# Optimization experiments

Measured on AMD Instinct MI355X. Metric: run time of the kernel, lower is better.

Reference implementation:

```python
import jax, jax.numpy as jnp
import numpy as np

EPS = 1e-12  # F.normalize default eps

def _l2norm(x, axis):
    n = jnp.maximum(jnp.linalg.norm(x, axis=axis, keepdims=True), EPS)
    return x / n

def setup_inputs() -> dict:
    key = jax.random.key(0)
    k1, k2 = jax.random.split(key)
    B, G, D, K = 256, 100, 768, 128
    h = jax.random.normal(k1, (B, G, D), dtype=jnp.float32)
    duplicate_pooling = jax.random.normal(k2, (G, D, K), dtype=jnp.float32)
    out_extrap = jnp.zeros((B, G, K), dtype=jnp.float32)
    return {"h": h, "duplicate_pooling": duplicate_pooling, "out_extrap": out_extrap}

def reference(h, duplicate_pooling, out_extrap):
    # normalize=True: L2-normalize each h[:, i, :] over feature dim (dim=1 of the
    # flattened [B, D] view == last axis), and each w_i = W[i] over dim=0 (the D axis).
    hn = _l2norm(h, axis=-1)                       # [B, G, D]
    wn = _l2norm(duplicate_pooling, axis=1)        # [G, D, K]
    # Fused grouped batched GEMM over all G groups at once.
    out = jnp.einsum('bgd,gdk->bgk', hn, wn)       # [B, G, K]
    return out
```

## Files before the change

### kernel.cpp

```cpp
#include <hip/hip_runtime.h>

#define Gn   100
#define Bn   256
#define Dn   768
#define Kn   128
#define LDP  40

typedef __attribute__((ext_vector_type(8))) short short8;
typedef __attribute__((ext_vector_type(4))) float f32x4;

__device__ inline unsigned short f2b(float f) {
  union { float f; unsigned u; } v; v.f = f;
  unsigned r = v.u + 0x7FFFu + ((v.u >> 16) & 1u);
  return (unsigned short)(r >> 16);
}

__global__ __launch_bounds__(256) void groupfc_kernel(
    const float* __restrict__ h, const float* __restrict__ W,
    float* __restrict__ out) {
  const int g    = blockIdx.z;
  const int mt   = blockIdx.x;
  const int nt   = blockIdx.y;
  const int t    = threadIdx.x;
  const int lane = t & 63;
  const int wave = t >> 6;
  const int wm   = wave >> 1, wn = wave & 1;

  __shared__ short Alds[2][64 * LDP];
  __shared__ short Blds[2][64 * LDP];
  __shared__ float AssqL[64];
  __shared__ float BssqL[4][64];

  f32x4 acc00 = {0.f,0.f,0.f,0.f};
  f32x4 acc01 = acc00, acc10 = acc00, acc11 = acc00;

  const int ar = t >> 2;
  const int ac = (t & 3) * 8;
  const float* aptr = h + ((size_t)(mt * 64 + ar) * Gn + g) * Dn + ac;
  const int bk = t & 63;
  const int bd = (t >> 6) * 8;
  const float* bptr = W + (size_t)g * (Dn * Kn) + (size_t)bd * Kn + nt * 64 + bk;

  const int quad = lane >> 4;
  const int koff = quad * 8;
  const int l15  = lane & 15;
  const int m0   = wm * 32 + l15;
  const int n0   = wn * 32 + l15;

  float assq = 0.f, bssq = 0.f;

  float4 a0 = *(const float4*)(aptr);
  float4 a1 = *(const float4*)(aptr + 4);
  float bv[8];
#pragma unroll
  for (int i = 0; i < 8; ++i) bv[i] = bptr[(size_t)i * Kn];

  for (int kc = 0; kc < 24; ++kc) {
    float4 na0, na1;
    float nbv[8];
    if (kc < 23) {
      const int d0 = (kc + 1) * 32;
      na0 = *(const float4*)(aptr + d0);
      na1 = *(const float4*)(aptr + d0 + 4);
#pragma unroll
      for (int i = 0; i < 8; ++i) nbv[i] = bptr[(size_t)(d0 + i) * Kn];
    }

    assq += a0.x*a0.x + a0.y*a0.y + a0.z*a0.z + a0.w*a0.w
          + a1.x*a1.x + a1.y*a1.y + a1.z*a1.z + a1.w*a1.w;
    union { unsigned short us[8]; short8 v; } pa;
    pa.us[0]=f2b(a0.x); pa.us[1]=f2b(a0.y); pa.us[2]=f2b(a0.z); pa.us[3]=f2b(a0.w);
    pa.us[4]=f2b(a1.x); pa.us[5]=f2b(a1.y); pa.us[6]=f2b(a1.z); pa.us[7]=f2b(a1.w);
    *(short8*)&Alds[kc & 1][ar * LDP + ac] = pa.v;

    union { unsigned short us[8]; short8 v; } pb;
#pragma unroll
    for (int i = 0; i < 8; ++i) { bssq += bv[i] * bv[i]; pb.us[i] = f2b(bv[i]); }
    *(short8*)&Blds[kc & 1][bk * LDP + bd] = pb.v;

    __syncthreads();

    short8 af0 = *(const short8*)&Alds[kc & 1][m0 * LDP + koff];
    short8 af1 = *(const short8*)&Alds[kc & 1][(m0 + 16) * LDP + koff];
    short8 bf0 = *(const short8*)&Blds[kc & 1][n0 * LDP + koff];
    short8 bf1 = *(const short8*)&Blds[kc & 1][(n0 + 16) * LDP + koff];

    acc00 = __builtin_amdgcn_mfma_f32_16x16x32_bf16(af0, bf0, acc00, 0, 0, 0);
    acc01 = __builtin_amdgcn_mfma_f32_16x16x32_bf16(af0, bf1, acc01, 0, 0, 0);
    acc10 = __builtin_amdgcn_mfma_f32_16x16x32_bf16(af1, bf0, acc10, 0, 0, 0);
    acc11 = __builtin_amdgcn_mfma_f32_16x16x32_bf16(af1, bf1, acc11, 0, 0, 0);

    a0 = na0; a1 = na1;
#pragma unroll
    for (int i = 0; i < 8; ++i) bv[i] = nbv[i];
  }

  assq += __shfl_xor(assq, 1);
  assq += __shfl_xor(assq, 2);
  if ((t & 3) == 0) AssqL[ar] = assq;
  BssqL[wave][bk] = bssq;
  __syncthreads();

  const float ws0 = BssqL[0][n0] + BssqL[1][n0] + BssqL[2][n0] + BssqL[3][n0];
  const float ws1 = BssqL[0][n0+16] + BssqL[1][n0+16] + BssqL[2][n0+16] + BssqL[3][n0+16];
  const float wi0 = 1.0f / fmaxf(sqrtf(ws0), 1e-12f);
  const float wi1 = 1.0f / fmaxf(sqrtf(ws1), 1e-12f);

#pragma unroll
  for (int mi = 0; mi < 2; ++mi) {
#pragma unroll
    for (int r = 0; r < 4; ++r) {
      const int lr  = wm * 32 + mi * 16 + quad * 4 + r;
      const float hs = 1.0f / fmaxf(sqrtf(AssqL[lr]), 1e-12f);
      const float v0 = (mi ? acc10[r] : acc00[r]) * hs * wi0;
      const float v1 = (mi ? acc11[r] : acc01[r]) * hs * wi1;
      const int row = mt * 64 + lr;
      const size_t ob = ((size_t)row * Gn + g) * Kn + nt * 64;
      out[ob + wn * 32 + l15]      = v0;
      out[ob + wn * 32 + l15 + 16] = v1;
    }
  }
}

extern "C" void kernel_launch(void* const* d_in, const int* in_sizes, int n_in,
                              void* d_out, int out_size, void* d_ws, size_t ws_size,
                              hipStream_t stream) {
  const float* h = (const float*)d_in[0];
  const float* W = (const float*)d_in[1];
  float* out = (float*)d_out;
  hipLaunchKernelGGL(groupfc_kernel, dim3(4, 2, Gn), dim3(256), 0, stream, h, W, out);
}
```

Baseline: 171.9 us.

## Deepen prefetch to two stages, triple-buffer LDS, remap blocks per XCD, cheaper bf16 pack

Global loads are now prefetched two K-chunks ahead into rotating register sets, and LDS is triple-buffered. The per-iteration __syncthreads is replaced by an LDS-only wait plus barrier, so outstanding global loads are not drained at each step. The grid is flattened and remapped so all 8 tiles of a group land on the same XCD for L2 reuse of W and h, with some idle blocks padding the grid. The bf16 conversion switches to round-half-up via a byte permute, which is slightly different rounding and more register pressure.

```diff
diff --git a/kernel.cpp b/kernel.cpp
--- a/kernel.cpp
+++ b/kernel.cpp
@@ -9,25 +9,35 @@
 typedef __attribute__((ext_vector_type(8))) short short8;
 typedef __attribute__((ext_vector_type(4))) float f32x4;
 
-__device__ inline unsigned short f2b(float f) {
-  union { float f; unsigned u; } v; v.f = f;
-  unsigned r = v.u + 0x7FFFu + ((v.u >> 16) & 1u);
-  return (unsigned short)(r >> 16);
+__device__ inline unsigned pack2(float lo, float hi) {
+  union { float f; unsigned u; } a, b; a.f = lo; b.f = hi;
+  return __builtin_amdgcn_perm(b.u + 0x8000u, a.u + 0x8000u, 0x07060302u);
+}
+
+__device__ inline void barrier_nodrain() {
+  asm volatile("s_waitcnt lgkmcnt(0)\n\ts_barrier" ::: "memory");
 }
 
 __global__ __launch_bounds__(256) void groupfc_kernel(
     const float* __restrict__ h, const float* __restrict__ W,
     float* __restrict__ out) {
-  const int g    = blockIdx.z;
-  const int mt   = blockIdx.x;
-  const int nt   = blockIdx.y;
+  const int id   = blockIdx.x;
+  const int xcd  = id & 7;
+  const int rest = id >> 3;
+  const int tl   = rest & 7;
+  const int g    = (rest >> 3) * 8 + xcd;
+  if (g >= Gn) return;
+  const int mt   = tl >> 1;
+  const int nt   = tl & 1;
+
   const int t    = threadIdx.x;
   const int lane = t & 63;
   const int wave = t >> 6;
   const int wm   = wave >> 1, wn = wave & 1;
+  const int l15  = lane & 15, quad = lane >> 4;
 
-  __shared__ short Alds[2][64 * LDP];
-  __shared__ short Blds[2][64 * LDP];
+  __shared__ __align__(16) short Af[3][64 * LDP];
+  __shared__ __align__(16) short Bf[3][64 * LDP];
   __shared__ float AssqL[64];
   __shared__ float BssqL[4][64];
 
@@ -38,67 +48,68 @@
   const int ac = (t & 3) * 8;
   const float* aptr = h + ((size_t)(mt * 64 + ar) * Gn + g) * Dn + ac;
   const int bk = t & 63;
-  const int bd = (t >> 6) * 8;
-  const float* bptr = W + (size_t)g * (Dn * Kn) + (size_t)bd * Kn + nt * 64 + bk;
+  const int bq = t >> 6;
+  const float* bptr = W + (size_t)g * (Dn * Kn) + (size_t)(bq * 8) * Kn + nt * 64 + bk;
 
-  const int quad = lane >> 4;
   const int koff = quad * 8;
-  const int l15  = lane & 15;
   const int m0   = wm * 32 + l15;
   const int n0   = wn * 32 + l15;
 
   float assq = 0.f, bssq = 0.f;
+  float4 Ar[2][2];
+  float  Br[2][8];
 
-  float4 a0 = *(const float4*)(aptr);
-  float4 a1 = *(const float4*)(aptr + 4);
-  float bv[8];
+  auto load_set = [&](int c, int s) {
+    const int d0 = c * 32;
+    Ar[s][0] = *(const float4*)(aptr + d0);
+    Ar[s][1] = *(const float4*)(aptr + d0 + 4);
 #pragma unroll
-  for (int i = 0; i < 8; ++i) bv[i] = bptr[(size_t)i * Kn];
+    for (int i = 0; i < 8; ++i) Br[s][i] = bptr[(size_t)(d0 + i) * Kn];
+  };
 
-  for (int kc = 0; kc < 24; ++kc) {
-    float4 na0, na1;
-    float nbv[8];
-    if (kc < 23) {
-      const int d0 = (kc + 1) * 32;
-      na0 = *(const float4*)(aptr + d0);
-      na1 = *(const float4*)(aptr + d0 + 4);
-#pragma unroll
-      for (int i = 0; i < 8; ++i) nbv[i] = bptr[(size_t)(d0 + i) * Kn];
-    }
-
+  auto pack_set = [&](int c, int s) {
+    const float4 a0 = Ar[s][0], a1 = Ar[s][1];
     assq += a0.x*a0.x + a0.y*a0.y + a0.z*a0.z + a0.w*a0.w
           + a1.x*a1.x + a1.y*a1.y + a1.z*a1.z + a1.w*a1.w;
-    union { unsigned short us[8]; short8 v; } pa;
-    pa.us[0]=f2b(a0.x); pa.us[1]=f2b(a0.y); pa.us[2]=f2b(a0.z); pa.us[3]=f2b(a0.w);
-    pa.us[4]=f2b(a1.x); pa.us[5]=f2b(a1.y); pa.us[6]=f2b(a1.z); pa.us[7]=f2b(a1.w);
-    *(short8*)&Alds[kc & 1][ar * LDP + ac] = pa.v;
+    uint4 ap;
+    ap.x = pack2(a0.x, a0.y); ap.y = pack2(a0.z, a0.w);
+    ap.z = pack2(a1.x, a1.y); ap.w = pack2(a1.z, a1.w);
+    *(uint4*)&Af[c % 3][ar * LDP + ac] = ap;
 
-    union { unsigned short us[8]; short8 v; } pb;
+    uint4 bp;
+    bp.x = pack2(Br[s][0], Br[s][1]); bp.y = pack2(Br[s][2], Br[s][3]);
+    bp.z = pack2(Br[s][4], Br[s][5]); bp.w = pack2(Br[s][6], Br[s][7]);
 #pragma unroll
-    for (int i = 0; i < 8; ++i) { bssq += bv[i] * bv[i]; pb.us[i] = f2b(bv[i]); }
-    *(short8*)&Blds[kc & 1][bk * LDP + bd] = pb.v;
+    for (int i = 0; i < 8; ++i) bssq += Br[s][i] * Br[s][i];
+    *(uint4*)&Bf[c % 3][bk * LDP + bq * 8] = bp;
+  };
 
-    __syncthreads();
+  load_set(0, 0);
+  load_set(1, 1);
+  pack_set(0, 0);
 
-    short8 af0 = *(const short8*)&Alds[kc & 1][m0 * LDP + koff];
-    short8 af1 = *(const short8*)&Alds[kc & 1][(m0 + 16) * LDP + koff];
-    short8 bf0 = *(const short8*)&Blds[kc & 1][n0 * LDP + koff];
-    short8 bf1 = *(const short8*)&Blds[kc & 1][(n0 + 16) * LDP + koff];
+#pragma unroll
+  for (int c = 0; c < 24; ++c) {
+    if (c + 2 < 24) load_set(c + 2, c & 1);
+    if (c + 1 < 24) pack_set(c + 1, (c + 1) & 1);
+    barrier_nodrain();
+
+    const int b = c % 3;
+    short8 af0 = *(const short8*)&Af[b][m0 * LDP + koff];
+    short8 af1 = *(const short8*)&Af[b][(m0 + 16) * LDP + koff];
+    short8 bf0 = *(const short8*)&Bf[b][n0 * LDP + koff];
+    short8 bf1 = *(const short8*)&Bf[b][(n0 + 16) * LDP + koff];
 
     acc00 = __builtin_amdgcn_mfma_f32_16x16x32_bf16(af0, bf0, acc00, 0, 0, 0);
     acc01 = __builtin_amdgcn_mfma_f32_16x16x32_bf16(af0, bf1, acc01, 0, 0, 0);
     acc10 = __builtin_amdgcn_mfma_f32_16x16x32_bf16(af1, bf0, acc10, 0, 0, 0);
     acc11 = __builtin_amdgcn_mfma_f32_16x16x32_bf16(af1, bf1, acc11, 0, 0, 0);
-
-    a0 = na0; a1 = na1;
-#pragma unroll
-    for (int i = 0; i < 8; ++i) bv[i] = nbv[i];
   }
 
   assq += __shfl_xor(assq, 1);
   assq += __shfl_xor(assq, 2);
   if ((t & 3) == 0) AssqL[ar] = assq;
-  BssqL[wave][bk] = bssq;
+  BssqL[bq][bk] = bssq;
   __syncthreads();
 
   const float ws0 = BssqL[0][n0] + BssqL[1][n0] + BssqL[2][n0] + BssqL[3][n0];
@@ -110,7 +121,7 @@
   for (int mi = 0; mi < 2; ++mi) {
 #pragma unroll
     for (int r = 0; r < 4; ++r) {
-      const int lr  = wm * 32 + mi * 16 + quad * 4 + r;
+      const int lr = wm * 32 + mi * 16 + quad * 4 + r;
       const float hs = 1.0f / fmaxf(sqrtf(AssqL[lr]), 1e-12f);
       const float v0 = (mi ? acc10[r] : acc00[r]) * hs * wi0;
       const float v1 = (mi ? acc11[r] : acc01[r]) * hs * wi1;
@@ -128,5 +139,5 @@
   const float* h = (const float*)d_in[0];
   const float* W = (const float*)d_in[1];
   float* out = (float*)d_out;
-  hipLaunchKernelGGL(groupfc_kernel, dim3(4, 2, Gn), dim3(256), 0, stream, h, W, out);
+  hipLaunchKernelGGL(groupfc_kernel, dim3(832), dim3(256), 0, stream, h, W, out);
 }
```

Result: no change. 169.5 us (-1.4%).
